# Optimization experiments

Measured on AMD Instinct MI355X. Metric: run time of the kernel, lower is better.

## Reference

```python
import jax, jax.numpy as jnp
import numpy as np

HIDDEN = 4096
N_HEADS = 32
N_KV_HEADS = 8
HEAD_DIM = 128
ROPE_THETA = 1e6
EPS = 1e-6
T = 2048


def setup_inputs() -> dict:
    key = jax.random.key(0)
    k1, k2, k3, k4, k5 = jax.random.split(key, 5)
    q_size = N_HEADS * HEAD_DIM
    kv_size = N_KV_HEADS * HEAD_DIM
    return {
        "positions": jnp.arange(T, dtype=jnp.int32),
        "hidden_states": jax.random.normal(k1, (T, HIDDEN), dtype=jnp.float32),
        "Wqkv": jax.random.normal(k2, (HIDDEN, q_size + 2 * kv_size), dtype=jnp.float32) * (HIDDEN ** -0.5),
        "Wo": jax.random.normal(k3, (q_size, HIDDEN), dtype=jnp.float32) * (q_size ** -0.5),
        "q_norm_w": jnp.ones((HEAD_DIM,), dtype=jnp.float32) + 0.01 * jax.random.normal(k4, (HEAD_DIM,), dtype=jnp.float32),
        "k_norm_w": jnp.ones((HEAD_DIM,), dtype=jnp.float32) + 0.01 * jax.random.normal(k5, (HEAD_DIM,), dtype=jnp.float32),
    }


def _rmsnorm(x, w):
    var = jnp.mean(jnp.square(x), axis=-1, keepdims=True)
    return x * jax.lax.rsqrt(var + EPS) * w


def _rope(x, positions):
    # NeoX-style rotate-half RoPE, rotary_dim == head_dim. x: [T, H, D]
    half = HEAD_DIM // 2
    inv_freq = 1.0 / (ROPE_THETA ** (jnp.arange(0, half, dtype=jnp.float32) / half))
    ang = positions.astype(jnp.float32)[:, None] * inv_freq  # [T, D/2]
    cos = jnp.cos(ang)[:, None, :]  # [T, 1, D/2]
    sin = jnp.sin(ang)[:, None, :]
    x1, x2 = x[..., :half], x[..., half:]
    return jnp.concatenate([x1 * cos - x2 * sin, x2 * cos + x1 * sin], axis=-1)


def reference(positions, hidden_states, Wqkv, Wo, q_norm_w, k_norm_w):
    q_size = N_HEADS * HEAD_DIM
    kv_size = N_KV_HEADS * HEAD_DIM
    qkv = hidden_states @ Wqkv  # [T, q+2kv]
    q = qkv[:, :q_size].reshape(-1, N_HEADS, HEAD_DIM)
    k = qkv[:, q_size:q_size + kv_size].reshape(-1, N_KV_HEADS, HEAD_DIM)
    v = qkv[:, q_size + kv_size:].reshape(-1, N_KV_HEADS, HEAD_DIM)
    q = _rmsnorm(q, q_norm_w)
    k = _rmsnorm(k, k_norm_w)
    q = _rope(q, positions)
    k = _rope(k, positions)
    rep = N_HEADS // N_KV_HEADS
    k = jnp.repeat(k, rep, axis=1)  # [T, 32, D]
    v = jnp.repeat(v, rep, axis=1)
    scale = HEAD_DIM ** -0.5
    scores = jnp.einsum('thd,shd->hts', q, k) * scale  # [H, T, T]
    t = hidden_states.shape[0]
    causal = jnp.tril(jnp.ones((t, t), dtype=bool))
    scores = jnp.where(causal[None, :, :], scores, jnp.finfo(scores.dtype).min)
    probs = jax.nn.softmax(scores, axis=-1)
    o = jnp.einsum('hts,shd->thd', probs, v)  # [T, H, D]
    return o.reshape(t, -1) @ Wo  # [T, hidden]
```

## Files before the change

### kernel.cpp

```cpp
#include <hip/hip_runtime.h>

#define T_SEQ 2048
#define HID   4096
#define NH    32
#define NKV   8
#define HD    128
#define QS    (NH*HD)
#define KVS   (NKV*HD)
#define QKVN  (QS + 2*KVS)

typedef unsigned short u16;
typedef __attribute__((ext_vector_type(8))) __bf16 bf16x8;
typedef __attribute__((ext_vector_type(8))) unsigned short u16x8;
typedef __attribute__((ext_vector_type(4))) unsigned short u16x4;
typedef __attribute__((ext_vector_type(4))) float f32x4;

__device__ __forceinline__ u16 f2bu(float x) {
  unsigned u = __builtin_bit_cast(unsigned, x);
  return (u16)((u + 0x7fffu + ((u >> 16) & 1u)) >> 16);
}
__device__ __forceinline__ float bu2f(u16 v) {
  unsigned u = ((unsigned)v) << 16;
  return __builtin_bit_cast(float, u);
}
__device__ __forceinline__ void gload16(const void* g, void* l) {
  __builtin_amdgcn_global_load_lds((const __attribute__((address_space(1))) void*)g,
                                   (__attribute__((address_space(3))) void*)l, 16, 0, 0);
}

__global__ void k_cvt(const float* __restrict__ in, u16* __restrict__ out, int n8) {
  for (int i = blockIdx.x * blockDim.x + threadIdx.x; i < n8; i += gridDim.x * blockDim.x) {
    const float4* p = (const float4*)in + (size_t)i * 2;
    float4 a = p[0], b = p[1];
    u16x8 v;
    v[0]=f2bu(a.x); v[1]=f2bu(a.y); v[2]=f2bu(a.z); v[3]=f2bu(a.w);
    v[4]=f2bu(b.x); v[5]=f2bu(b.y); v[6]=f2bu(b.z); v[7]=f2bu(b.w);
    *((u16x8*)out + i) = v;
  }
}

__global__ void k_transcvt(const float* __restrict__ in, u16* __restrict__ out, int R, int C) {
  __shared__ float tile[64][65];
  const int c0 = blockIdx.x * 64, r0 = blockIdx.y * 64;
  const int tid = threadIdx.x;
  const int row = tid >> 2, c4 = (tid & 3) * 4;
#pragma unroll
  for (int j = 0; j < 4; ++j) {
    float4 a = *(const float4*)(in + (size_t)(r0 + row) * C + c0 + c4 + j * 16);
    tile[row][c4 + j * 16 + 0] = a.x;
    tile[row][c4 + j * 16 + 1] = a.y;
    tile[row][c4 + j * 16 + 2] = a.z;
    tile[row][c4 + j * 16 + 3] = a.w;
  }
  __syncthreads();
  const int col = tid >> 2, rq = (tid & 3) * 16;
  u16x8 v0, v1;
#pragma unroll
  for (int j = 0; j < 8; ++j) v0[j] = f2bu(tile[rq + j][col]);
#pragma unroll
  for (int j = 0; j < 8; ++j) v1[j] = f2bu(tile[rq + 8 + j][col]);
  u16* dst = out + (size_t)(c0 + col) * R + r0 + rq;
  *(u16x8*)(dst) = v0;
  *(u16x8*)(dst + 8) = v1;
}

template<int OUTF32>
__global__ __launch_bounds__(256, 2)
void k_gemm(const u16* __restrict__ A, const u16* __restrict__ Bt,
            void* __restrict__ C, int K, int ldc) {
  __shared__ u16 sA[128 * 64];
  __shared__ u16 sB[128 * 64];
  const int tid = threadIdx.x;
  const int w = tid >> 6, lane = tid & 63, lo = lane & 15, hi = lane >> 4;
  const int wr = w >> 1, wc = w & 1;
  const int bm = blockIdx.y * 128, bn = blockIdx.x * 128;
  f32x4 acc[4][4] = {};
  const int nk = K >> 6;
  for (int kt = 0; kt < nk; ++kt) {
    const int kbase = kt * 64;
#pragma unroll
    for (int i = 0; i < 4; ++i) {
      int c = i * 256 + tid;
      int row = c >> 3, o8 = (c & 7) * 8;
      gload16(A + (size_t)(bm + row) * K + kbase + o8, sA + c * 8);
      gload16(Bt + (size_t)(bn + row) * K + kbase + o8, sB + c * 8);
    }
    __syncthreads();
#pragma unroll
    for (int kc = 0; kc < 2; ++kc) {
      bf16x8 af[4], bfr[4];
#pragma unroll
      for (int m = 0; m < 4; ++m)
        af[m] = *(const bf16x8*)(sA + (wr * 64 + m * 16 + lo) * 64 + kc * 32 + hi * 8);
#pragma unroll
      for (int n = 0; n < 4; ++n)
        bfr[n] = *(const bf16x8*)(sB + (wc * 64 + n * 16 + lo) * 64 + kc * 32 + hi * 8);
#pragma unroll
      for (int m = 0; m < 4; ++m)
#pragma unroll
        for (int n = 0; n < 4; ++n)
          acc[m][n] = __builtin_amdgcn_mfma_f32_16x16x32_bf16(af[m], bfr[n], acc[m][n], 0, 0, 0);
    }
    __syncthreads();
  }
#pragma unroll
  for (int m = 0; m < 4; ++m)
#pragma unroll
    for (int n = 0; n < 4; ++n) {
      int col = bn + wc * 64 + n * 16 + lo;
#pragma unroll
      for (int r = 0; r < 4; ++r) {
        int row = bm + wr * 64 + m * 16 + hi * 4 + r;
        float v = acc[m][n][r];
        if (OUTF32) ((float*)C)[(size_t)row * ldc + col] = v;
        else        ((u16*)C)[(size_t)row * ldc + col] = f2bu(v);
      }
    }
}

__global__ void k_normrope(const u16* __restrict__ qkv, const int* __restrict__ pos,
                           const float* __restrict__ qw, const float* __restrict__ kw,
                           u16* __restrict__ qb, u16* __restrict__ kb, u16* __restrict__ vb) {
  const int t = blockIdx.x;
  const int tid = threadIdx.x, w = tid >> 6, lane = tid & 63;
  const float p = (float)pos[t];
  const int d0 = lane * 2;
  const int j = d0 & 63;
  const float L2T_64 = 19.931568569324174f / 64.0f;
  float ang0 = p * exp2f(-(float)j * L2T_64);
  float ang1 = p * exp2f(-(float)(j + 1) * L2T_64);
  float c0 = cosf(ang0), s0 = sinf(ang0);
  float c1 = cosf(ang1), s1 = sinf(ang1);
  const bool hiHalf = lane >= 32;
  for (int it = 0; it < 10; ++it) {
    int h = it * 4 + w;
    bool isq = h < NH;
    int base = t * QKVN + (isq ? h * HD : QS + (h - NH) * HD);
    float x0 = bu2f(qkv[base + d0]);
    float x1 = bu2f(qkv[base + d0 + 1]);
    float ss = x0 * x0 + x1 * x1;
#pragma unroll
    for (int off = 1; off < 64; off <<= 1) ss += __shfl_xor(ss, off);
    float inv = rsqrtf(ss * (1.0f / 128.0f) + 1e-6f);
    const float* nw = isq ? qw : kw;
    float y0 = x0 * inv * nw[d0];
    float y1 = x1 * inv * nw[d0 + 1];
    float z0 = __shfl_xor(y0, 32);
    float z1 = __shfl_xor(y1, 32);
    float r0 = hiHalf ? (y0 * c0 + z0 * s0) : (y0 * c0 - z0 * s0);
    float r1 = hiHalf ? (y1 * c1 + z1 * s1) : (y1 * c1 - z1 * s1);
    u16* dst = isq ? (qb + ((size_t)h * T_SEQ + t) * HD)
                   : (kb + ((size_t)(h - NH) * T_SEQ + t) * HD);
    dst[d0] = f2bu(r0);
    dst[d0 + 1] = f2bu(r1);
  }
  for (int i = tid; i < KVS; i += 256) {
    int kvh = i >> 7, d = i & 127;
    vb[((size_t)kvh * T_SEQ + t) * HD + d] = qkv[t * QKVN + QS + KVS + i];
  }
}

__global__ __launch_bounds__(256, 4)
void k_attn(const u16* __restrict__ qb, const u16* __restrict__ kb,
            const u16* __restrict__ vb, u16* __restrict__ ao) {
  __shared__ u16 Ks[64 * 128];
  __shared__ u16 Vt[128 * 64];
  __shared__ u16 Ps[4][16 * 64];
  const int h = blockIdx.y, kvh = h >> 2;
  const int tid = threadIdx.x, w = tid >> 6, lane = tid & 63, lo = lane & 15, hi = lane >> 4;
  const int lo7 = lane & 7;
  const float scale = 0.08838834764831845f;
  const u16* Kb = kb + (size_t)kvh * T_SEQ * HD;
  const u16* Vb = vb + (size_t)kvh * T_SEQ * HD;
  const int krow = tid >> 4;
  const int kg = (tid & 15) ^ (krow & 7);
  const int vkvc = tid & 15, vfc = tid >> 4;

  for (int item = 0; item < 2; ++item) {
    const int xb = item == 0 ? blockIdx.x : 31 - blockIdx.x;
    const int q0 = xb * 64;
    const int nkt = xb + 1;
    const int qr0 = q0 + w * 16;
    bf16x8 qf[4];
    const u16* Qp = qb + ((size_t)h * T_SEQ + qr0 + lo) * HD;
#pragma unroll
    for (int kc = 0; kc < 4; ++kc) qf[kc] = *(const bf16x8*)(Qp + kc * 32 + hi * 8);
    f32x4 o[8] = {};
    float mrow[4], ssum[4];
#pragma unroll
    for (int r = 0; r < 4; ++r) { mrow[r] = -1e30f; ssum[r] = 0.f; }

    for (int kt = 0; kt < nkt; ++kt) {
#pragma unroll
      for (int i = 0; i < 4; ++i)
        gload16(Kb + (size_t)(kt * 64 + i * 16 + krow) * HD + kg * 8,
                Ks + i * 2048 + tid * 8);
      {
        u16x8 vv0 = *(const u16x8*)(Vb + (size_t)(kt * 64 + vkvc * 4 + 0) * HD + vfc * 8);
        u16x8 vv1 = *(const u16x8*)(Vb + (size_t)(kt * 64 + vkvc * 4 + 1) * HD + vfc * 8);
        u16x8 vv2 = *(const u16x8*)(Vb + (size_t)(kt * 64 + vkvc * 4 + 2) * HD + vfc * 8);
        u16x8 vv3 = *(const u16x8*)(Vb + (size_t)(kt * 64 + vkvc * 4 + 3) * HD + vfc * 8);
#pragma unroll
        for (int e = 0; e < 8; ++e) {
          int feat = vfc * 8 + e;
          int gp = (vkvc >> 1) ^ (feat & 7);
          u16x4 pk; pk[0] = vv0[e]; pk[1] = vv1[e]; pk[2] = vv2[e]; pk[3] = vv3[e];
          *(u16x4*)(Vt + feat * 64 + gp * 8 + (vkvc & 1) * 4) = pk;
        }
      }
      __syncthreads();
      f32x4 sa[4] = {};
#pragma unroll
      for (int kc = 0; kc < 4; ++kc) {
#pragma unroll
        for (int n = 0; n < 4; ++n) {
          int row = n * 16 + lo;
          bf16x8 kf = *(const bf16x8*)(Ks + row * 128 + (((kc * 4 + hi) ^ lo7) * 8));
          sa[n] = __builtin_amdgcn_mfma_f32_16x16x32_bf16(qf[kc], kf, sa[n], 0, 0, 0);
        }
      }
      float pvv[4][4], pmax[4];
#pragma unroll
      for (int r = 0; r < 4; ++r) {
        int qi = qr0 + hi * 4 + r;
        float pm = -1e30f;
#pragma unroll
        for (int n = 0; n < 4; ++n) {
          int kj = kt * 64 + n * 16 + lo;
          float sv = (kj <= qi) ? sa[n][r] * scale : -1e30f;
          pvv[n][r] = sv;
          pm = fmaxf(pm, sv);
        }
#pragma unroll
        for (int off = 1; off < 16; off <<= 1) pm = fmaxf(pm, __shfl_xor(pm, off));
        pmax[r] = pm;
      }
#pragma unroll
      for (int r = 0; r < 4; ++r) {
        float mnew = fmaxf(mrow[r], pmax[r]);
        float corr = __expf(mrow[r] - mnew);
        mrow[r] = mnew;
        float ps = 0.f;
#pragma unroll
        for (int n = 0; n < 4; ++n) {
          float p = __expf(pvv[n][r] - mnew);
          pvv[n][r] = p; ps += p;
        }
#pragma unroll
        for (int off = 1; off < 16; off <<= 1) ps += __shfl_xor(ps, off);
        ssum[r] = ssum[r] * corr + ps;
#pragma unroll
        for (int nf = 0; nf < 8; ++nf) o[nf][r] *= corr;
      }
      u16* Pw = Ps[w];
#pragma unroll
      for (int n = 0; n < 4; ++n) {
        int gcol = n * 2 + (lo >> 3);
#pragma unroll
        for (int r = 0; r < 4; ++r) {
          int row = hi * 4 + r;
          Pw[row * 64 + ((gcol ^ (row & 7)) * 8) + lo7] = f2bu(pvv[n][r]);
        }
      }
#pragma unroll
      for (int ks = 0; ks < 2; ++ks) {
        bf16x8 pf = *(const bf16x8*)(Pw + lo * 64 + (((ks * 4 + hi) ^ lo7) * 8));
#pragma unroll
        for (int nf = 0; nf < 8; ++nf) {
          int feat = nf * 16 + lo;
          bf16x8 vf = *(const bf16x8*)(Vt + feat * 64 + (((ks * 4 + hi) ^ lo7) * 8));
          o[nf] = __builtin_amdgcn_mfma_f32_16x16x32_bf16(pf, vf, o[nf], 0, 0, 0);
        }
      }
      __syncthreads();
    }
#pragma unroll
    for (int r = 0; r < 4; ++r) ssum[r] = 1.0f / ssum[r];
#pragma unroll
    for (int nf = 0; nf < 8; ++nf)
#pragma unroll
      for (int r = 0; r < 4; ++r) {
        int row = qr0 + hi * 4 + r;
        ao[(size_t)row * HID + h * HD + nf * 16 + lo] = f2bu(o[nf][r] * ssum[r]);
      }
  }
}

extern "C" void kernel_launch(void* const* d_in, const int* in_sizes, int n_in,
                              void* d_out, int out_size, void* d_ws, size_t ws_size,
                              hipStream_t stream) {
  (void)in_sizes; (void)n_in; (void)out_size; (void)ws_size;
  const int*   positions = (const int*)d_in[0];
  const float* hs   = (const float*)d_in[1];
  const float* wqkv = (const float*)d_in[2];
  const float* wo   = (const float*)d_in[3];
  const float* qnw  = (const float*)d_in[4];
  const float* knw  = (const float*)d_in[5];
  char* ws = (char*)d_ws;

  u16* hsb   = (u16*)d_out;
  u16* qbuf  = (u16*)d_out + 8388608;
  u16* wqkvT = (u16*)(ws + 0);
  u16* woT   = (u16*)(ws + 50331648);
  u16* qkvb  = (u16*)(ws + 83886080);
  u16* kbuf  = (u16*)(ws + 109051904);
  u16* vbuf  = (u16*)(ws + 113246208);
  u16* aob   = (u16*)(ws + 0);

  k_cvt<<<2048, 256, 0, stream>>>(hs, hsb, (T_SEQ * HID) / 8);
  k_transcvt<<<dim3(QKVN / 64, HID / 64), 256, 0, stream>>>(wqkv, wqkvT, HID, QKVN);
  k_transcvt<<<dim3(HID / 64, QS / 64), 256, 0, stream>>>(wo, woT, QS, HID);
  k_gemm<0><<<dim3(QKVN / 128, T_SEQ / 128), 256, 0, stream>>>(hsb, wqkvT, qkvb, HID, QKVN);
  k_normrope<<<T_SEQ, 256, 0, stream>>>(qkvb, positions, qnw, knw, qbuf, kbuf, vbuf);
  k_attn<<<dim3(16, NH), 256, 0, stream>>>(qbuf, kbuf, vbuf, aob);
  k_gemm<1><<<dim3(HID / 128, T_SEQ / 128), 256, 0, stream>>>(aob, woT, d_out, QS, HID);
}
```

Measured before the change: 593.4 us.

## Double-buffer K/V tiles in attention and merge conversion kernels into one launch

The attention kernel now double-buffers K and V tiles in shared memory. The next tile's K is issued via async global-to-LDS loads and its V is loaded into registers before the current tile's MFMAs, then transposed into the alternate buffer afterward, which removes one barrier per iteration. This roughly doubles LDS use and lowers the launch-bounds occupancy hint from 4 to 2 blocks. Separately, the hidden-state conversion and the two weight transpose-convert kernels are fused into a single k_prep launch to save launch overhead.

```diff
diff --git a/kernel.cpp b/kernel.cpp
--- a/kernel.cpp
+++ b/kernel.cpp
@@ -28,21 +28,28 @@
                                    (__attribute__((address_space(3))) void*)l, 16, 0, 0);
 }
 
-__global__ void k_cvt(const float* __restrict__ in, u16* __restrict__ out, int n8) {
-  for (int i = blockIdx.x * blockDim.x + threadIdx.x; i < n8; i += gridDim.x * blockDim.x) {
-    const float4* p = (const float4*)in + (size_t)i * 2;
-    float4 a = p[0], b = p[1];
-    u16x8 v;
-    v[0]=f2bu(a.x); v[1]=f2bu(a.y); v[2]=f2bu(a.z); v[3]=f2bu(a.w);
-    v[4]=f2bu(b.x); v[5]=f2bu(b.y); v[6]=f2bu(b.z); v[7]=f2bu(b.w);
-    *((u16x8*)out + i) = v;
-  }
-}
-
-__global__ void k_transcvt(const float* __restrict__ in, u16* __restrict__ out, int R, int C) {
+__global__ void k_prep(const float* __restrict__ hs, const float* __restrict__ wqkv,
+                       const float* __restrict__ wo, u16* __restrict__ hsb,
+                       u16* __restrict__ wqkvT, u16* __restrict__ woT) {
   __shared__ float tile[64][65];
-  const int c0 = blockIdx.x * 64, r0 = blockIdx.y * 64;
-  const int tid = threadIdx.x;
+  const int b = blockIdx.x, tid = threadIdx.x;
+  if (b < 2048) {
+    int i = b * 256 + tid;
+#pragma unroll
+    for (int g = 0; g < 2; ++g, i += 524288) {
+      const float4* p = (const float4*)hs + (size_t)i * 2;
+      float4 a = p[0], bb = p[1];
+      u16x8 v;
+      v[0]=f2bu(a.x); v[1]=f2bu(a.y); v[2]=f2bu(a.z); v[3]=f2bu(a.w);
+      v[4]=f2bu(bb.x); v[5]=f2bu(bb.y); v[6]=f2bu(bb.z); v[7]=f2bu(bb.w);
+      *((u16x8*)hsb + i) = v;
+    }
+    return;
+  }
+  const float* in; u16* out; int R, C, bx, by;
+  if (b < 8192) { in = wqkv; out = wqkvT; R = HID; C = QKVN; bx = (b - 2048) % 96; by = (b - 2048) / 96; }
+  else          { in = wo;   out = woT;   R = QS;  C = HID;  bx = (b - 8192) % 64; by = (b - 8192) / 64; }
+  const int c0 = bx * 64, r0 = by * 64;
   const int row = tid >> 2, c4 = (tid & 3) * 4;
 #pragma unroll
   for (int j = 0; j < 4; ++j) {
@@ -160,11 +167,11 @@
   }
 }
 
-__global__ __launch_bounds__(256, 4)
+__global__ __launch_bounds__(256, 2)
 void k_attn(const u16* __restrict__ qb, const u16* __restrict__ kb,
             const u16* __restrict__ vb, u16* __restrict__ ao) {
-  __shared__ u16 Ks[64 * 128];
-  __shared__ u16 Vt[128 * 64];
+  __shared__ u16 Ks[2][64 * 128];
+  __shared__ u16 Vt[2][128 * 64];
   __shared__ u16 Ps[4][16 * 64];
   const int h = blockIdx.y, kvh = h >> 2;
   const int tid = threadIdx.x, w = tid >> 6, lane = tid & 63, lo = lane & 15, hi = lane >> 4;
@@ -177,7 +184,7 @@
   const int vkvc = tid & 15, vfc = tid >> 4;
 
   for (int item = 0; item < 2; ++item) {
-    const int xb = item == 0 ? blockIdx.x : 31 - blockIdx.x;
+    const int xb = item == 0 ? (int)blockIdx.x : 31 - (int)blockIdx.x;
     const int q0 = xb * 64;
     const int nkt = xb + 1;
     const int qr0 = q0 + w * 16;
@@ -190,32 +197,41 @@
 #pragma unroll
     for (int r = 0; r < 4; ++r) { mrow[r] = -1e30f; ssum[r] = 0.f; }
 
+    u16x8 vv[4];
+#pragma unroll
+    for (int r4 = 0; r4 < 4; ++r4)
+      vv[r4] = *(const u16x8*)(Vb + (size_t)(vkvc * 4 + r4) * HD + vfc * 8);
+#pragma unroll
+    for (int i = 0; i < 4; ++i)
+      gload16(Kb + (size_t)(i * 16 + krow) * HD + kg * 8, Ks[0] + i * 2048 + tid * 8);
+#pragma unroll
+    for (int e = 0; e < 8; ++e) {
+      int feat = vfc * 8 + e;
+      int gp = (vkvc >> 1) ^ (feat & 7);
+      u16x4 pk; pk[0] = vv[0][e]; pk[1] = vv[1][e]; pk[2] = vv[2][e]; pk[3] = vv[3][e];
+      *(u16x4*)(Vt[0] + feat * 64 + gp * 8 + (vkvc & 1) * 4) = pk;
+    }
+    __syncthreads();
+
     for (int kt = 0; kt < nkt; ++kt) {
-#pragma unroll
-      for (int i = 0; i < 4; ++i)
-        gload16(Kb + (size_t)(kt * 64 + i * 16 + krow) * HD + kg * 8,
-                Ks + i * 2048 + tid * 8);
-      {
-        u16x8 vv0 = *(const u16x8*)(Vb + (size_t)(kt * 64 + vkvc * 4 + 0) * HD + vfc * 8);
-        u16x8 vv1 = *(const u16x8*)(Vb + (size_t)(kt * 64 + vkvc * 4 + 1) * HD + vfc * 8);
-        u16x8 vv2 = *(const u16x8*)(Vb + (size_t)(kt * 64 + vkvc * 4 + 2) * HD + vfc * 8);
-        u16x8 vv3 = *(const u16x8*)(Vb + (size_t)(kt * 64 + vkvc * 4 + 3) * HD + vfc * 8);
-#pragma unroll
-        for (int e = 0; e < 8; ++e) {
-          int feat = vfc * 8 + e;
-          int gp = (vkvc >> 1) ^ (feat & 7);
-          u16x4 pk; pk[0] = vv0[e]; pk[1] = vv1[e]; pk[2] = vv2[e]; pk[3] = vv3[e];
-          *(u16x4*)(Vt + feat * 64 + gp * 8 + (vkvc & 1) * 4) = pk;
-        }
-      }
-      __syncthreads();
+      const int cur = kt & 1;
+      const bool pf = (kt + 1 < nkt);
+      if (pf) {
+#pragma unroll
+        for (int r4 = 0; r4 < 4; ++r4)
+          vv[r4] = *(const u16x8*)(Vb + (size_t)((kt + 1) * 64 + vkvc * 4 + r4) * HD + vfc * 8);
+#pragma unroll
+        for (int i = 0; i < 4; ++i)
+          gload16(Kb + (size_t)((kt + 1) * 64 + i * 16 + krow) * HD + kg * 8,
+                  Ks[cur ^ 1] + i * 2048 + tid * 8);
+      }
       f32x4 sa[4] = {};
 #pragma unroll
       for (int kc = 0; kc < 4; ++kc) {
 #pragma unroll
         for (int n = 0; n < 4; ++n) {
           int row = n * 16 + lo;
-          bf16x8 kf = *(const bf16x8*)(Ks + row * 128 + (((kc * 4 + hi) ^ lo7) * 8));
+          bf16x8 kf = *(const bf16x8*)(Ks[cur] + row * 128 + (((kc * 4 + hi) ^ lo7) * 8));
           sa[n] = __builtin_amdgcn_mfma_f32_16x16x32_bf16(qf[kc], kf, sa[n], 0, 0, 0);
         }
       }
@@ -264,12 +280,21 @@
       }
 #pragma unroll
       for (int ks = 0; ks < 2; ++ks) {
-        bf16x8 pf = *(const bf16x8*)(Pw + lo * 64 + (((ks * 4 + hi) ^ lo7) * 8));
+        bf16x8 pfr = *(const bf16x8*)(Pw + lo * 64 + (((ks * 4 + hi) ^ lo7) * 8));
 #pragma unroll
         for (int nf = 0; nf < 8; ++nf) {
           int feat = nf * 16 + lo;
-          bf16x8 vf = *(const bf16x8*)(Vt + feat * 64 + (((ks * 4 + hi) ^ lo7) * 8));
-          o[nf] = __builtin_amdgcn_mfma_f32_16x16x32_bf16(pf, vf, o[nf], 0, 0, 0);
+          bf16x8 vf = *(const bf16x8*)(Vt[cur] + feat * 64 + (((ks * 4 + hi) ^ lo7) * 8));
+          o[nf] = __builtin_amdgcn_mfma_f32_16x16x32_bf16(pfr, vf, o[nf], 0, 0, 0);
+        }
+      }
+      if (pf) {
+#pragma unroll
+        for (int e = 0; e < 8; ++e) {
+          int feat = vfc * 8 + e;
+          int gp = (vkvc >> 1) ^ (feat & 7);
+          u16x4 pk; pk[0] = vv[0][e]; pk[1] = vv[1][e]; pk[2] = vv[2][e]; pk[3] = vv[3][e];
+          *(u16x4*)(Vt[cur ^ 1] + feat * 64 + gp * 8 + (vkvc & 1) * 4) = pk;
         }
       }
       __syncthreads();
@@ -307,9 +332,7 @@
   u16* vbuf  = (u16*)(ws + 113246208);
   u16* aob   = (u16*)(ws + 0);
 
-  k_cvt<<<2048, 256, 0, stream>>>(hs, hsb, (T_SEQ * HID) / 8);
-  k_transcvt<<<dim3(QKVN / 64, HID / 64), 256, 0, stream>>>(wqkv, wqkvT, HID, QKVN);
-  k_transcvt<<<dim3(HID / 64, QS / 64), 256, 0, stream>>>(wo, woT, QS, HID);
+  k_prep<<<12288, 256, 0, stream>>>(hs, wqkv, wo, hsb, wqkvT, woT);
   k_gemm<0><<<dim3(QKVN / 128, T_SEQ / 128), 256, 0, stream>>>(hsb, wqkvT, qkvb, HID, QKVN);
   k_normrope<<<T_SEQ, 256, 0, stream>>>(qkvb, positions, qnw, knw, qbuf, kbuf, vbuf);
   k_attn<<<dim3(16, NH), 256, 0, stream>>>(qbuf, kbuf, vbuf, aob);
```

After: 563.3 us. -5.1%, faster.
